# Kernel tuning notes

Hardware: AMD Instinct MI355X
Metric: run time of the kernel (lower is better)

## Reference

```python
import jax, jax.numpy as jnp
import numpy as np

N_NODES = 100000
N_EDGES = 640000
HIDDEN = 128
IN_DIM = 4


def setup_inputs() -> dict:
    key = jax.random.key(0)
    ks = jax.random.split(key, 8)
    x = jax.random.normal(ks[0], (N_NODES, IN_DIM), dtype=jnp.float32)
    edge_index = jax.random.randint(ks[1], (2, N_EDGES), 0, N_NODES, dtype=jnp.int32)
    edge_attr = jax.random.uniform(ks[2], (N_EDGES,), dtype=jnp.float32)
    # PyG GraphConv params: lin_rel (with bias) applied to aggregated messages,
    # lin_root (no bias) applied to the node's own features.
    W1_rel = jax.random.normal(ks[3], (IN_DIM, HIDDEN), dtype=jnp.float32) * 0.5
    b1 = jnp.zeros((HIDDEN,), dtype=jnp.float32)
    W1_root = jax.random.normal(ks[4], (IN_DIM, HIDDEN), dtype=jnp.float32) * 0.5
    W2_rel = jax.random.normal(ks[5], (HIDDEN, 1), dtype=jnp.float32) * 0.1
    b2 = jnp.zeros((1,), dtype=jnp.float32)
    W2_root = jax.random.normal(ks[6], (HIDDEN, 1), dtype=jnp.float32) * 0.1
    return {
        "x": x, "edge_index": edge_index, "edge_attr": edge_attr,
        "W1_rel": W1_rel, "b1": b1, "W1_root": W1_root,
        "W2_rel": W2_rel, "b2": b2, "W2_root": W2_root,
    }


def _graph_conv(x, src, dst, edge_w, W_rel, b_rel, W_root):
    # message: edge_w * x[src]; aggregate: scatter-add at dst; then linear.
    msg = x[src] * edge_w[:, None]                      # [E, F]
    agg = jax.ops.segment_sum(msg, dst, num_segments=N_NODES)  # [N, F]
    return agg @ W_rel + b_rel + x @ W_root             # [N, out]


def reference(x, edge_index, edge_attr, W1_rel, b1, W1_root, W2_rel, b2, W2_root):
    src, dst = edge_index[0], edge_index[1]
    h = jax.nn.relu(_graph_conv(x, src, dst, edge_attr, W1_rel, b1, W1_root))
    out = _graph_conv(h, src, dst, edge_attr, W2_rel, b2, W2_root)
    return out
```

## Files before the change

kernel.cpp:

```cpp
#include <hip/hip_runtime.h>

#define N_NODES 100000
#define N_EDGES 640000
#define HIDDEN  128

#define NB    200
#define NBKT  500
#define PB    250
#define PT    256
#define EPT   10
#define BLK_RECS (PT * EPT)
#define RUNOF_CAP 2560

__global__ __launch_bounds__(PT) void partition_kernel(
    const int* __restrict__ ei, const float* __restrict__ ea,
    const float* __restrict__ W1_rel, const float* __restrict__ b1,
    const float* __restrict__ W1_root, const float* __restrict__ W2_rel,
    const float* __restrict__ W2_root,
    uint2* __restrict__ recs, int* __restrict__ bs,
    float* __restrict__ packed) {
    const int tid = threadIdx.x;
    const int pb  = blockIdx.x;

    if (pb == 0 && tid < HIDDEN) {
        float* p = packed + tid * 12;
#pragma unroll
        for (int k = 0; k < 4; ++k) p[k]     = W1_rel[k * HIDDEN + tid];
#pragma unroll
        for (int k = 0; k < 4; ++k) p[4 + k] = W1_root[k * HIDDEN + tid];
        p[8]  = b1[tid];
        p[9]  = W2_rel[tid];
        p[10] = W2_root[tid];
        p[11] = 0.f;
    }

    __shared__ int   hist[NBKT];
    __shared__ int   start[NBKT];
    __shared__ int   wcur[NBKT];
    __shared__ uint2 srec[BLK_RECS];

    for (int i = tid; i < NBKT; i += PT) hist[i] = 0;
    __syncthreads();

    int   dsts[EPT];
    int   srcs[EPT];
    float wts[EPT];
    const int e0 = pb * BLK_RECS + tid;
#pragma unroll
    for (int k = 0; k < EPT; ++k) {
        int e = e0 + k * PT;
        srcs[k] = ei[e];
        dsts[k] = ei[N_EDGES + e];
        wts[k]  = ea[e];
        atomicAdd(&hist[dsts[k] / NB], 1);
    }
    __syncthreads();

    if (tid < 64) {
        int base = 0;
        for (int c = 0; c < NBKT; c += 64) {
            int idx = c + tid;
            int v = (idx < NBKT) ? hist[idx] : 0;
            int orig = v;
#pragma unroll
            for (int off = 1; off < 64; off <<= 1) {
                int t = __shfl_up(v, off);
                if (tid >= off) v += t;
            }
            if (idx < NBKT) {
                start[idx] = base + v - orig;
                wcur[idx]  = base + v - orig;
            }
            base += __shfl(v, 63);
        }
    }
    __syncthreads();

    for (int i = tid; i < NBKT; i += PT) bs[i * PB + pb] = start[i];
    if (tid == 0) bs[NBKT * PB + pb] = BLK_RECS;

#pragma unroll
    for (int k = 0; k < EPT; ++k) {
        int d  = dsts[k];
        int b  = d / NB;
        int dl = d - b * NB;
        int slot = atomicAdd(&wcur[b], 1);
        srec[slot] = make_uint2((unsigned)srcs[k] | ((unsigned)dl << 17),
                                __float_as_uint(wts[k]));
    }
    __syncthreads();

    uint2* dst = recs + (size_t)pb * BLK_RECS;
    for (int j = tid; j < BLK_RECS; j += PT) dst[j] = srec[j];
}

__device__ __forceinline__ int find_run(const int* pfx, int f) {
    int lo = 0, hi = PB;
    while (hi - lo > 1) {
        int m = (lo + hi) >> 1;
        if (pfx[m] <= f) lo = m; else hi = m;
    }
    return lo;
}

__device__ __forceinline__ int build_runs(const int* __restrict__ bs, int b,
                                          int* rbase, int* pfx,
                                          short* run_of) {
    const int tid = threadIdx.x;
    __shared__ int lenA[PB];
    if (tid < PB) {
        int s = bs[b * PB + tid];
        int e = bs[(b + 1) * PB + tid];
        rbase[tid] = tid * BLK_RECS + s;
        lenA[tid]  = e - s;
    }
    __syncthreads();
    if (tid < 64) {
        int base = 0;
        for (int c = 0; c < PB; c += 64) {
            int idx = c + tid;
            int v = (idx < PB) ? lenA[idx] : 0;
            int orig = v;
#pragma unroll
            for (int off = 1; off < 64; off <<= 1) {
                int t = __shfl_up(v, off);
                if (tid >= off) v += t;
            }
            if (idx < PB) pfx[idx] = base + v - orig;
            base += __shfl(v, 63);
        }
        if (tid == 0) pfx[PB] = base;
    }
    __syncthreads();
    if (tid < PB) {
        int s = pfx[tid];
        int e = pfx[tid + 1];
        if (e > RUNOF_CAP) e = RUNOF_CAP;
        for (int j = s; j < e; ++j) run_of[j] = (short)tid;
    }
    __syncthreads();
    return pfx[PB];
}

__global__ __launch_bounds__(256) void fused_kernel(
    const uint2* __restrict__ recs, const int* __restrict__ bs,
    const float* __restrict__ x, const float* __restrict__ packed,
    const float* __restrict__ b2, float* __restrict__ s_rel,
    float* __restrict__ out) {
    __shared__ float accf[NB * 4];
    __shared__ int   rbase[PB];
    __shared__ int   pfx[PB + 1];
    __shared__ short run_of[RUNOF_CAP];

    const int tid = threadIdx.x;
    const int b   = blockIdx.x;

    for (int i = tid; i < NB * 4; i += 256) accf[i] = 0.f;
    const int cnt = build_runs(bs, b, rbase, pfx, run_of);

    for (int f = tid; f < cnt; f += 256) {
        int run = (f < RUNOF_CAP) ? (int)run_of[f] : find_run(pfx, f);
        uint2 rec = recs[(size_t)rbase[run] + (f - pfx[run])];
        int src = rec.x & 0x1FFFF;
        int dl  = rec.x >> 17;
        float w = __uint_as_float(rec.y);
        float4 xv = reinterpret_cast<const float4*>(x)[src];
        atomicAdd(&accf[dl * 4 + 0], xv.x * w);
        atomicAdd(&accf[dl * 4 + 1], xv.y * w);
        atomicAdd(&accf[dl * 4 + 2], xv.z * w);
        atomicAdd(&accf[dl * 4 + 3], xv.w * w);
    }
    __syncthreads();

    if (tid >= NB) return;
    const int n = b * NB + tid;

    float4 xv = reinterpret_cast<const float4*>(x)[n];
    float4 av = make_float4(accf[tid * 4 + 0], accf[tid * 4 + 1],
                            accf[tid * 4 + 2], accf[tid * 4 + 3]);

    const float4* pw = reinterpret_cast<const float4*>(packed);
    float srel = 0.f, sroot = 0.f;
#pragma unroll 4
    for (int j = 0; j < HIDDEN; ++j) {
        float4 wr = pw[j * 3 + 0];
        float4 wo = pw[j * 3 + 1];
        float4 wb = pw[j * 3 + 2];
        float pre = wb.x
                  + av.x * wr.x + av.y * wr.y + av.z * wr.z + av.w * wr.w
                  + xv.x * wo.x + xv.y * wo.y + xv.z * wo.z + xv.w * wo.w;
        float h = fmaxf(pre, 0.f);
        srel  += h * wb.y;
        sroot += h * wb.z;
    }
    s_rel[n] = srel;
    out[n]   = sroot + b2[0];
}

__global__ __launch_bounds__(256) void agg2_kernel(
    const uint2* __restrict__ recs, const int* __restrict__ bs,
    const float* __restrict__ s_rel, float* __restrict__ out) {
    __shared__ float acc[NB];
    __shared__ int   rbase[PB];
    __shared__ int   pfx[PB + 1];
    __shared__ short run_of[RUNOF_CAP];

    const int tid = threadIdx.x;
    const int b   = blockIdx.x;

    for (int i = tid; i < NB; i += 256) acc[i] = 0.f;
    const int cnt = build_runs(bs, b, rbase, pfx, run_of);

    for (int f = tid; f < cnt; f += 256) {
        int run = (f < RUNOF_CAP) ? (int)run_of[f] : find_run(pfx, f);
        uint2 rec = recs[(size_t)rbase[run] + (f - pfx[run])];
        int src = rec.x & 0x1FFFF;
        int dl  = rec.x >> 17;
        atomicAdd(&acc[dl], s_rel[src] * __uint_as_float(rec.y));
    }
    __syncthreads();

    if (tid < NB)
        out[b * NB + tid] += acc[tid];
}

__global__ void prep_legacy(const float* __restrict__ W1_rel,
                            const float* __restrict__ b1,
                            const float* __restrict__ W1_root,
                            const float* __restrict__ W2_rel,
                            const float* __restrict__ W2_root,
                            float* __restrict__ packed) {
    int t = threadIdx.x;
    if (t < HIDDEN) {
        float* p = packed + t * 12;
#pragma unroll
        for (int k = 0; k < 4; ++k) p[k]     = W1_rel[k * HIDDEN + t];
#pragma unroll
        for (int k = 0; k < 4; ++k) p[4 + k] = W1_root[k * HIDDEN + t];
        p[8]  = b1[t];
        p[9]  = W2_rel[t];
        p[10] = W2_root[t];
        p[11] = 0.f;
    }
}

__global__ void scatter1_legacy(const int* __restrict__ ei, const float* __restrict__ ea,
                                const float* __restrict__ x, float* __restrict__ agg) {
    int e = blockIdx.x * blockDim.x + threadIdx.x;
    if (e >= N_EDGES) return;
    int src = ei[e], dst = ei[N_EDGES + e];
    float w = ea[e];
    float4 xv = reinterpret_cast<const float4*>(x)[src];
    atomicAdd(&agg[dst * 4 + 0], xv.x * w);
    atomicAdd(&agg[dst * 4 + 1], xv.y * w);
    atomicAdd(&agg[dst * 4 + 2], xv.z * w);
    atomicAdd(&agg[dst * 4 + 3], xv.w * w);
}

__global__ __launch_bounds__(256) void node_legacy(const float* __restrict__ x,
                            const float* __restrict__ agg,
                            const float* __restrict__ packed,
                            const float* __restrict__ b2,
                            float* __restrict__ s_rel,
                            float* __restrict__ out) {
    int n = blockIdx.x * blockDim.x + threadIdx.x;
    if (n >= N_NODES) return;
    float4 xv = reinterpret_cast<const float4*>(x)[n];
    float4 av = reinterpret_cast<const float4*>(agg)[n];
    const float4* pw = reinterpret_cast<const float4*>(packed);
    float srel = 0.f, sroot = 0.f;
#pragma unroll 4
    for (int j = 0; j < HIDDEN; ++j) {
        float4 wr = pw[j * 3 + 0];
        float4 wo = pw[j * 3 + 1];
        float4 wb = pw[j * 3 + 2];
        float pre = wb.x
                  + av.x * wr.x + av.y * wr.y + av.z * wr.z + av.w * wr.w
                  + xv.x * wo.x + xv.y * wo.y + xv.z * wo.z + xv.w * wo.w;
        float h = fmaxf(pre, 0.f);
        srel  += h * wb.y;
        sroot += h * wb.z;
    }
    s_rel[n] = srel;
    out[n]   = sroot + b2[0];
}

__global__ void scatter2_legacy(const int* __restrict__ ei, const float* __restrict__ ea,
                                const float* __restrict__ s_rel, float* __restrict__ out) {
    int e = blockIdx.x * blockDim.x + threadIdx.x;
    if (e >= N_EDGES) return;
    atomicAdd(&out[ei[N_EDGES + e]], s_rel[ei[e]] * ea[e]);
}

extern "C" void kernel_launch(void* const* d_in, const int* in_sizes, int n_in,
                              void* d_out, int out_size, void* d_ws, size_t ws_size,
                              hipStream_t stream) {
    const float* x       = (const float*)d_in[0];
    const int*   ei      = (const int*)  d_in[1];
    const float* ea      = (const float*)d_in[2];
    const float* W1_rel  = (const float*)d_in[3];
    const float* b1      = (const float*)d_in[4];
    const float* W1_root = (const float*)d_in[5];
    const float* W2_rel  = (const float*)d_in[6];
    const float* b2      = (const float*)d_in[7];
    const float* W2_root = (const float*)d_in[8];
    float* out = (float*)d_out;
    char*  ws  = (char*)d_ws;

    float* packed = (float*)ws;
    float* s_rel  = packed + 1536;
    int*   bs     = (int*)(s_rel + N_NODES);
    uint2* recs   = (uint2*)(bs + (NBKT + 1) * PB);
    const size_t need = 1536 * 4 + (size_t)N_NODES * 4 +
                        (size_t)(NBKT + 1) * PB * 4 + (size_t)N_EDGES * 8;

    if (ws_size >= need) {
        partition_kernel<<<PB, PT, 0, stream>>>(ei, ea, W1_rel, b1, W1_root,
                                                W2_rel, W2_root, recs, bs, packed);
        fused_kernel<<<NBKT, 256, 0, stream>>>(recs, bs, x, packed, b2, s_rel, out);
        agg2_kernel<<<NBKT, 256, 0, stream>>>(recs, bs, s_rel, out);
    } else {
        float* agg = (float*)recs;
        dim3 grdE((N_EDGES + 255) / 256);
        dim3 grdN((N_NODES + 255) / 256);
        prep_legacy<<<1, 256, 0, stream>>>(W1_rel, b1, W1_root, W2_rel, W2_root, packed);
        hipMemsetAsync(agg, 0, (size_t)N_NODES * 4 * sizeof(float), stream);
        scatter1_legacy<<<grdE, 256, 0, stream>>>(ei, ea, x, agg);
        node_legacy<<<grdN, 256, 0, stream>>>(x, agg, packed, b2, s_rel, out);
        scatter2_legacy<<<grdE, 256, 0, stream>>>(ei, ea, s_rel, out);
    }
}
```

Baseline: 53.68 us.

## Double block size and batch three gathers per thread for memory-level parallelism

Raises the thread count of all three kernels to 512, halving edges per thread in the partition kernel. In the aggregation kernels each thread first issues up to three record loads, then three feature gathers, then the shared-memory atomics, so more loads are in flight before any result is used. The aim is to hide gather latency in a latency-bound scatter. It relies on build_runs and the prefix scan still working with 512 threads, and uses run_of without the cap check on the first three slots, which is safe only because those indices stay below RUNOF_CAP.

```diff
diff --git a/kernel.cpp b/kernel.cpp
--- a/kernel.cpp
+++ b/kernel.cpp
@@ -7,9 +7,10 @@
 #define NB    200
 #define NBKT  500
 #define PB    250
-#define PT    256
-#define EPT   10
+#define PT    512
+#define EPT   5
 #define BLK_RECS (PT * EPT)
+#define CT    512
 #define RUNOF_CAP 2560
 
 __global__ __launch_bounds__(PT) void partition_kernel(
@@ -142,7 +143,7 @@
     return pfx[PB];
 }
 
-__global__ __launch_bounds__(256) void fused_kernel(
+__global__ __launch_bounds__(CT) void fused_kernel(
     const uint2* __restrict__ recs, const int* __restrict__ bs,
     const float* __restrict__ x, const float* __restrict__ packed,
     const float* __restrict__ b2, float* __restrict__ s_rel,
@@ -155,12 +156,44 @@
     const int tid = threadIdx.x;
     const int b   = blockIdx.x;
 
-    for (int i = tid; i < NB * 4; i += 256) accf[i] = 0.f;
+    for (int i = tid; i < NB * 4; i += CT) accf[i] = 0.f;
     const int cnt = build_runs(bs, b, rbase, pfx, run_of);
 
-    for (int f = tid; f < cnt; f += 256) {
-        int run = (f < RUNOF_CAP) ? (int)run_of[f] : find_run(pfx, f);
-        uint2 rec = recs[(size_t)rbase[run] + (f - pfx[run])];
+    const int f0 = tid, f1 = tid + CT, f2 = tid + 2 * CT;
+    uint2 r0, r1, r2;
+    if (f0 < cnt) { int rn = run_of[f0]; r0 = recs[(size_t)rbase[rn] + (f0 - pfx[rn])]; }
+    if (f1 < cnt) { int rn = run_of[f1]; r1 = recs[(size_t)rbase[rn] + (f1 - pfx[rn])]; }
+    if (f2 < cnt) { int rn = run_of[f2]; r2 = recs[(size_t)rbase[rn] + (f2 - pfx[rn])]; }
+
+    float4 xv0, xv1, xv2;
+    if (f0 < cnt) xv0 = reinterpret_cast<const float4*>(x)[r0.x & 0x1FFFF];
+    if (f1 < cnt) xv1 = reinterpret_cast<const float4*>(x)[r1.x & 0x1FFFF];
+    if (f2 < cnt) xv2 = reinterpret_cast<const float4*>(x)[r2.x & 0x1FFFF];
+
+    if (f0 < cnt) {
+        int dl = r0.x >> 17; float w = __uint_as_float(r0.y);
+        atomicAdd(&accf[dl * 4 + 0], xv0.x * w);
+        atomicAdd(&accf[dl * 4 + 1], xv0.y * w);
+        atomicAdd(&accf[dl * 4 + 2], xv0.z * w);
+        atomicAdd(&accf[dl * 4 + 3], xv0.w * w);
+    }
+    if (f1 < cnt) {
+        int dl = r1.x >> 17; float w = __uint_as_float(r1.y);
+        atomicAdd(&accf[dl * 4 + 0], xv1.x * w);
+        atomicAdd(&accf[dl * 4 + 1], xv1.y * w);
+        atomicAdd(&accf[dl * 4 + 2], xv1.z * w);
+        atomicAdd(&accf[dl * 4 + 3], xv1.w * w);
+    }
+    if (f2 < cnt) {
+        int dl = r2.x >> 17; float w = __uint_as_float(r2.y);
+        atomicAdd(&accf[dl * 4 + 0], xv2.x * w);
+        atomicAdd(&accf[dl * 4 + 1], xv2.y * w);
+        atomicAdd(&accf[dl * 4 + 2], xv2.z * w);
+        atomicAdd(&accf[dl * 4 + 3], xv2.w * w);
+    }
+    for (int f = tid + 3 * CT; f < cnt; f += CT) {
+        int rn = (f < RUNOF_CAP) ? (int)run_of[f] : find_run(pfx, f);
+        uint2 rec = recs[(size_t)rbase[rn] + (f - pfx[rn])];
         int src = rec.x & 0x1FFFF;
         int dl  = rec.x >> 17;
         float w = __uint_as_float(rec.y);
@@ -197,7 +230,7 @@
     out[n]   = sroot + b2[0];
 }
 
-__global__ __launch_bounds__(256) void agg2_kernel(
+__global__ __launch_bounds__(CT) void agg2_kernel(
     const uint2* __restrict__ recs, const int* __restrict__ bs,
     const float* __restrict__ s_rel, float* __restrict__ out) {
     __shared__ float acc[NB];
@@ -208,15 +241,28 @@
     const int tid = threadIdx.x;
     const int b   = blockIdx.x;
 
-    for (int i = tid; i < NB; i += 256) acc[i] = 0.f;
+    for (int i = tid; i < NB; i += CT) acc[i] = 0.f;
     const int cnt = build_runs(bs, b, rbase, pfx, run_of);
 
-    for (int f = tid; f < cnt; f += 256) {
-        int run = (f < RUNOF_CAP) ? (int)run_of[f] : find_run(pfx, f);
-        uint2 rec = recs[(size_t)rbase[run] + (f - pfx[run])];
-        int src = rec.x & 0x1FFFF;
-        int dl  = rec.x >> 17;
-        atomicAdd(&acc[dl], s_rel[src] * __uint_as_float(rec.y));
+    const int f0 = tid, f1 = tid + CT, f2 = tid + 2 * CT;
+    uint2 r0, r1, r2;
+    if (f0 < cnt) { int rn = run_of[f0]; r0 = recs[(size_t)rbase[rn] + (f0 - pfx[rn])]; }
+    if (f1 < cnt) { int rn = run_of[f1]; r1 = recs[(size_t)rbase[rn] + (f1 - pfx[rn])]; }
+    if (f2 < cnt) { int rn = run_of[f2]; r2 = recs[(size_t)rbase[rn] + (f2 - pfx[rn])]; }
+
+    float s0 = 0.f, s1 = 0.f, s2 = 0.f;
+    if (f0 < cnt) s0 = s_rel[r0.x & 0x1FFFF];
+    if (f1 < cnt) s1 = s_rel[r1.x & 0x1FFFF];
+    if (f2 < cnt) s2 = s_rel[r2.x & 0x1FFFF];
+
+    if (f0 < cnt) atomicAdd(&acc[r0.x >> 17], s0 * __uint_as_float(r0.y));
+    if (f1 < cnt) atomicAdd(&acc[r1.x >> 17], s1 * __uint_as_float(r1.y));
+    if (f2 < cnt) atomicAdd(&acc[r2.x >> 17], s2 * __uint_as_float(r2.y));
+
+    for (int f = tid + 3 * CT; f < cnt; f += CT) {
+        int rn = (f < RUNOF_CAP) ? (int)run_of[f] : find_run(pfx, f);
+        uint2 rec = recs[(size_t)rbase[rn] + (f - pfx[rn])];
+        atomicAdd(&acc[rec.x >> 17], s_rel[rec.x & 0x1FFFF] * __uint_as_float(rec.y));
     }
     __syncthreads();
 
@@ -317,8 +363,8 @@
     if (ws_size >= need) {
         partition_kernel<<<PB, PT, 0, stream>>>(ei, ea, W1_rel, b1, W1_root,
                                                 W2_rel, W2_root, recs, bs, packed);
-        fused_kernel<<<NBKT, 256, 0, stream>>>(recs, bs, x, packed, b2, s_rel, out);
-        agg2_kernel<<<NBKT, 256, 0, stream>>>(recs, bs, s_rel, out);
+        fused_kernel<<<NBKT, CT, 0, stream>>>(recs, bs, x, packed, b2, s_rel, out);
+        agg2_kernel<<<NBKT, CT, 0, stream>>>(recs, bs, s_rel, out);
     } else {
         float* agg = (float*)recs;
         dim3 grdE((N_EDGES + 255) / 256);
```

Measured after the change: 53.25 us. About the same (-0.8%).

## Compact per-bucket edge records for second aggregation and transpose bucket offsets

Applied to the files above, without the earlier changes.

The first aggregation kernel now writes each bucket's gathered records contiguously into a compacted buffer along with a per-bucket count, so the second aggregation reads them linearly instead of rebuilding run prefix sums. The bucket-start table is transposed to a row per partition block, and partition and aggregation kernels move to 512 threads with 5 edges per thread. This removes the duplicated run setup and scattered record reads in the second pass, at the cost of an extra write of about 5 MB in the first pass and more workspace. Buckets over the cap fall back to the old run-based path.

```diff
diff --git a/kernel.cpp b/kernel.cpp
--- a/kernel.cpp
+++ b/kernel.cpp
@@ -7,17 +7,20 @@
 #define NB    200
 #define NBKT  500
 #define PB    250
-#define PT    256
-#define EPT   10
+#define PT    512
+#define EPT   5
 #define BLK_RECS (PT * EPT)
+#define CT    512
 #define RUNOF_CAP 2560
+#define CAP2  2048
+#define BSROW (NBKT + 1)
 
 __global__ __launch_bounds__(PT) void partition_kernel(
     const int* __restrict__ ei, const float* __restrict__ ea,
     const float* __restrict__ W1_rel, const float* __restrict__ b1,
     const float* __restrict__ W1_root, const float* __restrict__ W2_rel,
     const float* __restrict__ W2_root,
-    uint2* __restrict__ recs, int* __restrict__ bs,
+    uint2* __restrict__ recs, int* __restrict__ bs_t,
     float* __restrict__ packed) {
     const int tid = threadIdx.x;
     const int pb  = blockIdx.x;
@@ -76,8 +79,8 @@
     }
     __syncthreads();
 
-    for (int i = tid; i < NBKT; i += PT) bs[i * PB + pb] = start[i];
-    if (tid == 0) bs[NBKT * PB + pb] = BLK_RECS;
+    for (int i = tid; i < NBKT; i += PT) bs_t[pb * BSROW + i] = start[i];
+    if (tid == 0) bs_t[pb * BSROW + NBKT] = BLK_RECS;
 
 #pragma unroll
     for (int k = 0; k < EPT; ++k) {
@@ -103,14 +106,27 @@
     return lo;
 }
 
-__device__ __forceinline__ int build_runs(const int* __restrict__ bs, int b,
-                                          int* rbase, int* pfx,
-                                          short* run_of) {
+__global__ __launch_bounds__(CT) void fused_kernel(
+    const uint2* __restrict__ recs, const int* __restrict__ bs_t,
+    const float* __restrict__ x, const float* __restrict__ packed,
+    const float* __restrict__ b2, float* __restrict__ s_rel,
+    float* __restrict__ out, uint2* __restrict__ crecs,
+    int* __restrict__ cnts) {
+    __shared__ float accf[NB * 4];
+    __shared__ int   rbase[PB];
+    __shared__ int   lenA[PB];
+    __shared__ int   pfx[PB + 1];
+    __shared__ short run_of[RUNOF_CAP];
+
     const int tid = threadIdx.x;
-    __shared__ int lenA[PB];
+    const int b   = blockIdx.x;
+
+    for (int i = tid; i < NB * 4; i += CT) accf[i] = 0.f;
+
     if (tid < PB) {
-        int s = bs[b * PB + tid];
-        int e = bs[(b + 1) * PB + tid];
+        const int* row = bs_t + tid * BSROW;
+        int s = row[b];
+        int e = row[b + 1];
         rbase[tid] = tid * BLK_RECS + s;
         lenA[tid]  = e - s;
     }
@@ -132,6 +148,8 @@
         if (tid == 0) pfx[PB] = base;
     }
     __syncthreads();
+    const int cnt = pfx[PB];
+    if (tid == 0) cnts[b] = cnt;
     if (tid < PB) {
         int s = pfx[tid];
         int e = pfx[tid + 1];
@@ -139,28 +157,11 @@
         for (int j = s; j < e; ++j) run_of[j] = (short)tid;
     }
     __syncthreads();
-    return pfx[PB];
-}
-
-__global__ __launch_bounds__(256) void fused_kernel(
-    const uint2* __restrict__ recs, const int* __restrict__ bs,
-    const float* __restrict__ x, const float* __restrict__ packed,
-    const float* __restrict__ b2, float* __restrict__ s_rel,
-    float* __restrict__ out) {
-    __shared__ float accf[NB * 4];
-    __shared__ int   rbase[PB];
-    __shared__ int   pfx[PB + 1];
-    __shared__ short run_of[RUNOF_CAP];
-
-    const int tid = threadIdx.x;
-    const int b   = blockIdx.x;
-
-    for (int i = tid; i < NB * 4; i += 256) accf[i] = 0.f;
-    const int cnt = build_runs(bs, b, rbase, pfx, run_of);
-
-    for (int f = tid; f < cnt; f += 256) {
-        int run = (f < RUNOF_CAP) ? (int)run_of[f] : find_run(pfx, f);
-        uint2 rec = recs[(size_t)rbase[run] + (f - pfx[run])];
+
+    for (int f = tid; f < cnt; f += CT) {
+        int rn = (f < RUNOF_CAP) ? (int)run_of[f] : find_run(pfx, f);
+        uint2 rec = recs[(size_t)rbase[rn] + (f - pfx[rn])];
+        if (f < CAP2) crecs[(size_t)b * CAP2 + f] = rec;
         int src = rec.x & 0x1FFFF;
         int dl  = rec.x >> 17;
         float w = __uint_as_float(rec.y);
@@ -197,26 +198,61 @@
     out[n]   = sroot + b2[0];
 }
 
-__global__ __launch_bounds__(256) void agg2_kernel(
-    const uint2* __restrict__ recs, const int* __restrict__ bs,
+__global__ __launch_bounds__(CT) void agg2_kernel(
+    const uint2* __restrict__ recs, const int* __restrict__ bs_t,
+    const uint2* __restrict__ crecs, const int* __restrict__ cnts,
     const float* __restrict__ s_rel, float* __restrict__ out) {
     __shared__ float acc[NB];
-    __shared__ int   rbase[PB];
-    __shared__ int   pfx[PB + 1];
-    __shared__ short run_of[RUNOF_CAP];
 
     const int tid = threadIdx.x;
     const int b   = blockIdx.x;
 
-    for (int i = tid; i < NB; i += 256) acc[i] = 0.f;
-    const int cnt = build_runs(bs, b, rbase, pfx, run_of);
-
-    for (int f = tid; f < cnt; f += 256) {
-        int run = (f < RUNOF_CAP) ? (int)run_of[f] : find_run(pfx, f);
-        uint2 rec = recs[(size_t)rbase[run] + (f - pfx[run])];
-        int src = rec.x & 0x1FFFF;
-        int dl  = rec.x >> 17;
-        atomicAdd(&acc[dl], s_rel[src] * __uint_as_float(rec.y));
+    for (int i = tid; i < NB; i += CT) acc[i] = 0.f;
+    const int cnt = cnts[b];
+    __syncthreads();
+
+    if (cnt <= CAP2) {
+        const uint2* r = crecs + (size_t)b * CAP2;
+        for (int f = tid; f < cnt; f += CT) {
+            uint2 rec = r[f];
+            atomicAdd(&acc[rec.x >> 17],
+                      s_rel[rec.x & 0x1FFFF] * __uint_as_float(rec.y));
+        }
+    } else {
+        __shared__ int rbase[PB];
+        __shared__ int lenA[PB];
+        __shared__ int pfx[PB + 1];
+        if (tid < PB) {
+            const int* row = bs_t + tid * BSROW;
+            int s = row[b];
+            int e = row[b + 1];
+            rbase[tid] = tid * BLK_RECS + s;
+            lenA[tid]  = e - s;
+        }
+        __syncthreads();
+        if (tid < 64) {
+            int base = 0;
+            for (int c = 0; c < PB; c += 64) {
+                int idx = c + tid;
+                int v = (idx < PB) ? lenA[idx] : 0;
+                int orig = v;
+#pragma unroll
+                for (int off = 1; off < 64; off <<= 1) {
+                    int t = __shfl_up(v, off);
+                    if (tid >= off) v += t;
+                }
+                if (idx < PB) pfx[idx] = base + v - orig;
+                base += __shfl(v, 63);
+            }
+            if (tid == 0) pfx[PB] = base;
+        }
+        __syncthreads();
+        for (int f = tid; f < cnt; f += CT) {
+            int rn = find_run(pfx, f);
+            uint2 rec = recs[(size_t)rbase[rn] + (f - pfx[rn])];
+            atomicAdd(&acc[rec.x >> 17],
+                      s_rel[rec.x & 0x1FFFF] * __uint_as_float(rec.y));
+        }
     }
     __syncthreads();
 
@@ -309,16 +345,20 @@
 
     float* packed = (float*)ws;
     float* s_rel  = packed + 1536;
-    int*   bs     = (int*)(s_rel + N_NODES);
-    uint2* recs   = (uint2*)(bs + (NBKT + 1) * PB);
-    const size_t need = 1536 * 4 + (size_t)N_NODES * 4 +
-                        (size_t)(NBKT + 1) * PB * 4 + (size_t)N_EDGES * 8;
+    int*   cnts   = (int*)(s_rel + N_NODES);
+    int*   bs_t   = cnts + NBKT;
+    uint2* recs   = (uint2*)(bs_t + PB * BSROW);
+    uint2* crecs  = recs + (size_t)N_EDGES;
+    const size_t need = 1536 * 4 + (size_t)N_NODES * 4 + NBKT * 4 +
+                        (size_t)PB * BSROW * 4 + (size_t)N_EDGES * 8 +
+                        (size_t)NBKT * CAP2 * 8;
 
     if (ws_size >= need) {
         partition_kernel<<<PB, PT, 0, stream>>>(ei, ea, W1_rel, b1, W1_root,
-                                                W2_rel, W2_root, recs, bs, packed);
-        fused_kernel<<<NBKT, 256, 0, stream>>>(recs, bs, x, packed, b2, s_rel, out);
-        agg2_kernel<<<NBKT, 256, 0, stream>>>(recs, bs, s_rel, out);
+                                                W2_rel, W2_root, recs, bs_t, packed);
+        fused_kernel<<<NBKT, CT, 0, stream>>>(recs, bs_t, x, packed, b2,
+                                              s_rel, out, crecs, cnts);
+        agg2_kernel<<<NBKT, CT, 0, stream>>>(recs, bs_t, crecs, cnts, s_rel, out);
     } else {
         float* agg = (float*)recs;
         dim3 grdE((N_EDGES + 255) / 256);
```

New measurement: 45.95 us, median of 2. 1.17x faster.
